# Performance work log

Measured on AMD Instinct MI355X. Metric: run time of the kernel, lower is better.

The kernel has to match this reference:

```python
import jax, jax.numpy as jnp
import numpy as np


def setup_inputs() -> dict:
    key = jax.random.key(0)
    k1, k2 = jax.random.split(key, 2)
    B, N, D = 8, 2048, 1024
    x = jax.random.normal(k1, (B, N, D), dtype=jnp.float32)
    # Linear(D, 3D): weight stored as [in, out] for x @ W
    W_qkv = jax.random.normal(k2, (D, 3 * D), dtype=jnp.float32) * (D ** -0.5)
    b_qkv = jnp.zeros((3 * D,), dtype=jnp.float32)
    return {"x": x, "W_qkv": W_qkv, "b_qkv": b_qkv}


def reference(x, W_qkv, b_qkv):
    D = x.shape[-1]
    scale = D ** -0.5
    qkv = x @ W_qkv + b_qkv                      # [B, N, 3D]
    q, k, v = jnp.split(qkv, 3, axis=-1)         # each [B, N, D]
    # attention scores: note original scales AFTER matmul (same math)
    atten = jnp.einsum('bnd,bmd->bnm', q, k) * scale  # [B, N, N]
    atten = jax.nn.softmax(atten, axis=-1)
    out = jnp.einsum('bnm,bmd->bnd', atten, v)   # [B, N, D]
    return out
```

## Files before the change

kernel.cpp:

```cpp
#include <hip/hip_runtime.h>
#include <hip/hip_bf16.h>


typedef __attribute__((ext_vector_type(8))) short bf16x8;
typedef __attribute__((ext_vector_type(4))) float f32x4;
typedef __attribute__((ext_vector_type(8))) unsigned short u16x8;
typedef __attribute__((address_space(1))) const unsigned int gu32;
typedef __attribute__((address_space(3))) unsigned int lu32;

__device__ __forceinline__ unsigned short f2bf(float f) {
  union { float f; unsigned int u; } v; v.f = f;
  unsigned int r = v.u + 0x7fffu + ((v.u >> 16) & 1u);
  return (unsigned short)(r >> 16);
}
__device__ __forceinline__ void cp16(const unsigned short* g, unsigned short* l) {
  __builtin_amdgcn_global_load_lds((gu32*)g, (lu32*)l, 16, 0, 0);
}

__global__ __launch_bounds__(256) void prep(const float* __restrict__ x,
                                            unsigned short* __restrict__ xb,
                                            const float* __restrict__ W,
                                            unsigned short* __restrict__ Wt,
                                            float* __restrict__ rowsum) {
  __shared__ unsigned short tile[64][72];
  int bid = blockIdx.x, t = threadIdx.x;
  if (bid < 8192) {
    long i = ((long)bid * 256 + t) * 8;
    float4 a = *(const float4*)(x + i);
    float4 b = *(const float4*)(x + i + 4);
    u16x8 o;
    o[0] = f2bf(a.x); o[1] = f2bf(a.y); o[2] = f2bf(a.z); o[3] = f2bf(a.w);
    o[4] = f2bf(b.x); o[5] = f2bf(b.y); o[6] = f2bf(b.z); o[7] = f2bf(b.w);
    *(u16x8*)(xb + i) = o;
  } else if (bid < 8960) {
    int wb = bid - 8192;
    int fb = wb % 48, db = wb / 48;
#pragma unroll
    for (int it = 0; it < 4; it++) {
      int c = t + it * 256;
      int r = c >> 4, c4 = (c & 15) * 4;
      float4 v = *(const float4*)(W + (long)(db * 64 + r) * 3072 + fb * 64 + c4);
      tile[r][c4 + 0] = f2bf(v.x); tile[r][c4 + 1] = f2bf(v.y);
      tile[r][c4 + 2] = f2bf(v.z); tile[r][c4 + 3] = f2bf(v.w);
    }
    __syncthreads();
#pragma unroll
    for (int it = 0; it < 2; it++) {
      int c = t + it * 256;
      int r2 = c >> 3, k8 = (c & 7) * 8;
      u16x8 o;
#pragma unroll
      for (int j = 0; j < 8; j++) o[j] = tile[k8 + j][r2];
      *(u16x8*)(Wt + (long)(fb * 64 + r2) * 1024 + db * 64 + k8) = o;
    }
  } else {
    rowsum[(bid - 8960) * 256 + t] = 0.f;
  }
}

template <int MODE, int SWZ>
__global__ __launch_bounds__(512, 2) void gemm256(
    const unsigned short* __restrict__ A, const unsigned short* __restrict__ B,
    float* __restrict__ C, const float* __restrict__ bias, int Ncols, int K, float scale,
    unsigned short* __restrict__ qp, unsigned short* __restrict__ kp,
    unsigned short* __restrict__ vp, float* __restrict__ rsum,
    long strA, long strB, long strC) {
  __shared__ __align__(16) unsigned short smem[4][256 * 64];
  const int tid = threadIdx.x;
  const int lane = tid & 63, wave = tid >> 6;
  const int quad = lane >> 4, l16 = lane & 15;
  const int lr = lane >> 3, lc = lane & 7;
  const int bz = blockIdx.z;
  int mt, nt;
  {
    int bid = blockIdx.x;
    const int nx = gridDim.x;
    bid = (bid & 7) * (nx >> 3) + (bid >> 3);
    int w = bid & 15, st = bid >> 4;
    constexpr int NSUP = (SWZ >= 4) ? (SWZ / 4) : 1;
    mt = (st / NSUP) * 4 + (w >> 2);
    nt = (st % NSUP) * 4 + (w & 3);
  }
  const long m0 = (long)mt * 256;
  const int n0 = nt * 256;
  const int wm128 = (wave >> 2) * 128;
  const int wn64 = (wave & 3) * 64;
  const int NT = K >> 6, mask = NT - 1;

  const unsigned short* __restrict__ Ab = A + (long)bz * strA;
  const unsigned short* __restrict__ Bb = B + (long)bz * strB;

  unsigned int aSrc[4], bSrc[4];
  int aOff[4], bOff[4];
  {
    const int auL[4] = {0, 128, 64, 192}, auH[4] = {32, 160, 96, 224};
    const int buL[4] = {0, 128, 32, 160}, buH[4] = {64, 192, 96, 224};
    const bool wlo = wave < 4;
    const int w8 = (wave & 3) * 8;
    const int sc = (lc ^ lr) * 8;
#pragma unroll
    for (int u = 0; u < 4; u++) {
      int ra = (wlo ? auL[u] : auH[u]) + w8 + lr;
      int rb = (wlo ? buL[u] : buH[u]) + w8 + lr;
      aSrc[u] = (unsigned int)(((int)m0 + ra) * K + sc);
      bSrc[u] = (unsigned int)((n0 + rb) * K + sc);
      aOff[u] = ra * 64 + lc * 8;
      bOff[u] = rb * 64 + lc * 8;
    }
  }

#define SA(u, bb, tt) cp16(Ab + aSrc[u] + (tt) * 64, &smem[bb][aOff[u]])
#define SB(u, bb, tt) cp16(Bb + bSrc[u] + (tt) * 64, &smem[2 + (bb)][bOff[u]])

  f32x4 acc[8][4];
  f32x4 zero = {0.f, 0.f, 0.f, 0.f};
#pragma unroll
  for (int i = 0; i < 8; i++)
#pragma unroll
    for (int j = 0; j < 4; j++) acc[i][j] = zero;
  bf16x8 am[2][2][2];
  bf16x8 bn[4][2];

#define RD_AQ(d, bb, q)                                                                     \
  _Pragma("unroll") for (int ii = 0; ii < 2; ii++) {                                        \
    int row = wm128 + ((q) * 2 + ii) * 16 + l16;                                            \
    _Pragma("unroll") for (int h = 0; h < 2; h++)                                           \
      am[d][ii][h] = *(const bf16x8*)(&smem[bb][row * 64 + ((((h << 2) | quad)) ^ (row & 7)) * 8]); \
  }
#define RD_BALL(bb)                                                                         \
  _Pragma("unroll") for (int jj = 0; jj < 4; jj++) {                                        \
    int row = wn64 + jj * 16 + l16;                                                         \
    _Pragma("unroll") for (int h = 0; h < 2; h++)                                           \
      bn[jj][h] = *(const bf16x8*)(&smem[2 + (bb)][row * 64 + ((((h << 2) | quad)) ^ (row & 7)) * 8]); \
  }
#define MMQ(q, d)                                                                           \
  _Pragma("unroll") for (int ii = 0; ii < 2; ii++)                                          \
    _Pragma("unroll") for (int jj = 0; jj < 4; jj++)                                        \
      _Pragma("unroll") for (int h = 0; h < 2; h++)                                         \
        acc[(q) * 2 + ii][jj] = __builtin_amdgcn_mfma_f32_16x16x32_bf16(                    \
            am[d][ii][h], bn[jj][h], acc[(q) * 2 + ii][jj], 0, 0, 0);
#define ABAR asm volatile("s_barrier" ::: "memory")
#define LGKM0 asm volatile("s_waitcnt lgkmcnt(0)" ::: "memory")
#define VMCNT4 asm volatile("s_waitcnt vmcnt(4)" ::: "memory")
#define PRIO1 __builtin_amdgcn_s_setprio(1)
#define PRIO0 __builtin_amdgcn_s_setprio(0)
#define SBAR0 __builtin_amdgcn_sched_barrier(0)

#define TILE(bb, tt)                                                                        \
  {                                                                                         \
    const int t2c_ = (tt) + 2;                                                              \
    const int t2_ = t2c_ > mask ? mask : t2c_;                                              \
                                                                                    \
    LGKM0; RD_AQ(1, bb, 1); ABAR;                                                           \
    SB(0, bb, t2_); SB(1, bb, t2_);                                                         \
    SBAR0; PRIO1; MMQ(0, 0); PRIO0; SBAR0;                                                  \
                                                                                    \
    LGKM0; RD_AQ(0, bb, 2); ABAR;                                                           \
    SA(0, bb, t2_); SA(1, bb, t2_);                                                         \
    SBAR0; PRIO1; MMQ(1, 1); PRIO0; SBAR0;                                                  \
                                                                                    \
    LGKM0; RD_AQ(1, bb, 3); VMCNT4; ABAR;                                                   \
    SB(2, bb, t2_); SB(3, bb, t2_);                                                         \
    SBAR0; PRIO1; MMQ(2, 0); PRIO0; SBAR0;                                                  \
                                                                                    \
    LGKM0; RD_AQ(0, (bb) ^ 1, 0);                                                           \
    SBAR0; PRIO1; MMQ(3, 1); PRIO0; SBAR0;                                                  \
    RD_BALL((bb) ^ 1);                                                                      \
    ABAR;                                                                                   \
    SA(2, bb, t2_); SA(3, bb, t2_);                                                         \
  }

  SA(0, 0, 0); SA(1, 0, 0); SB(0, 0, 0); SB(1, 0, 0);
  SA(2, 0, 0); SA(3, 0, 0); SB(2, 0, 0); SB(3, 0, 0);
  SA(0, 1, 1); SA(1, 1, 1); SB(0, 1, 1); SB(1, 1, 1);
  SA(2, 1, 1); SA(3, 1, 1); SB(2, 1, 1); SB(3, 1, 1);
  asm volatile("s_waitcnt vmcnt(8)" ::: "memory");
  ABAR;
  RD_AQ(0, 0, 0);
  RD_BALL(0);

#pragma unroll 1
  for (int t = 0; t < NT; t += 2) {
    TILE(0, t);
    TILE(1, t + 1);
  }

  if (MODE == 1 || MODE == 3) {
    asm volatile("s_waitcnt vmcnt(0)" ::: "memory");
    __syncthreads();
    unsigned short* Cs = &smem[0][0];
    if (MODE == 1) {
      float bv[4];
#pragma unroll
      for (int j = 0; j < 4; j++) bv[j] = bias[n0 + wn64 + j * 16 + l16];
      const bool isV = (n0 >= 2048);
#pragma unroll
      for (int i = 0; i < 8; i++)
#pragma unroll
        for (int r = 0; r < 4; r++) {
          int rw = wm128 + i * 16 + quad * 4 + r;
#pragma unroll
          for (int j = 0; j < 4; j++) {
            int cl = wn64 + j * 16 + l16;
            unsigned short hv = f2bf(acc[i][j][r] + bv[j]);
            int row = isV ? cl : rw, col = isV ? rw : cl;
            *(unsigned short*)((char*)Cs + ((row * 512 + col * 2) ^ ((row & 7) << 4))) = hv;
          }
        }
    } else {
      float* rs = rsum + bz * 2048;
#pragma unroll
      for (int i = 0; i < 8; i++)
#pragma unroll
        for (int r = 0; r < 4; r++) {
          int rw = wm128 + i * 16 + quad * 4 + r;
          float psum = 0.f;
#pragma unroll
          for (int j = 0; j < 4; j++) {
            float e = __expf(acc[i][j][r] * scale);
            psum += e;
            int col = wn64 + j * 16 + l16;
            *(unsigned short*)((char*)Cs + ((rw * 512 + col * 2) ^ ((rw & 7) << 4))) = f2bf(e);
          }
          psum += __shfl_xor(psum, 1);
          psum += __shfl_xor(psum, 2);
          psum += __shfl_xor(psum, 4);
          psum += __shfl_xor(psum, 8);
          if (l16 == 0) atomicAdd(rs + (m0 + rw), psum);
        }
    }
    __syncthreads();
    const int rrow = tid >> 5, rchunk = tid & 31;
    unsigned short* dst;
    long rowstr, rowbase, colbase;
    if (MODE == 3) {
      dst = qp + (long)bz * strC;
      rowstr = Ncols; rowbase = m0; colbase = n0;
    } else if (n0 < 2048) {
      dst = (n0 < 1024) ? qp : kp;
      rowstr = 1024; rowbase = m0; colbase = n0 & 1023;
    } else {
      dst = vp;
      rowstr = 2048; rowbase = (m0 >> 11) * 1024 + (n0 - 2048); colbase = m0 & 2047;
    }
#pragma unroll
    for (int k = 0; k < 16; k++) {
      int row = k * 16 + rrow;
      u16x8 v = *(const u16x8*)((char*)Cs + ((row * 512 + rchunk * 16) ^ ((row & 7) << 4)));
      *(u16x8*)(dst + (rowbase + row) * rowstr + colbase + rchunk * 8) = v;
    }
  } else {
    float* Co = C + (long)bz * strC;
    const float* rs = rsum + bz * 2048;
#pragma unroll
    for (int i = 0; i < 8; i++)
#pragma unroll
      for (int r = 0; r < 4; r++) {
        long gm = m0 + wm128 + i * 16 + quad * 4 + r;
        float inv = 1.0f / rs[gm];
#pragma unroll
        for (int j = 0; j < 4; j++)
          Co[gm * Ncols + n0 + wn64 + j * 16 + l16] = acc[i][j][r] * inv;
      }
  }
  asm volatile("s_waitcnt vmcnt(0) lgkmcnt(0)" ::: "memory");
#undef SA
#undef SB
#undef RD_AQ
#undef RD_BALL
#undef MMQ
#undef TILE
#undef ABAR
#undef LGKM0
#undef VMCNT4
#undef PRIO1
#undef PRIO0
#undef SBAR0
}

extern "C" void kernel_launch(void* const* d_in, const int* in_sizes, int n_in,
                              void* d_out, int out_size, void* d_ws, size_t ws_size,
                              hipStream_t stream) {
  const float* x = (const float*)d_in[0];
  const float* W = (const float*)d_in[1];
  const float* bq = (const float*)d_in[2];
  float* out = (float*)d_out;
  char* ws = (char*)d_ws;
  const long MB = 1L << 20;
  unsigned short* Q  = (unsigned short*)(ws);
  unsigned short* Kb = (unsigned short*)(ws + 32 * MB);
  unsigned short* Vt = (unsigned short*)(ws + 64 * MB);
  unsigned short* xb = (unsigned short*)(ws + 96 * MB);
  unsigned short* Wt = (unsigned short*)(ws + 128 * MB);
  unsigned short* E  = (unsigned short*)(ws + 96 * MB);
  float* rowsum      = (float*)(ws + 160 * MB);

  prep<<<9024, 256, 0, stream>>>(x, xb, W, Wt, rowsum);
  gemm256<1, 12><<<dim3(768, 1, 1), 512, 0, stream>>>(xb, Wt, nullptr, bq, 3072, 1024, 1.0f,
                                                      Q, Kb, Vt, nullptr, 0, 0, 0);
  gemm256<3, 8><<<dim3(64, 1, 8), 512, 0, stream>>>(Q, Kb, nullptr, nullptr, 2048, 1024,
                                                    0.03125f, E, nullptr, nullptr, rowsum,
                                                    2048L * 1024, 2048L * 1024, 2048L * 2048);
  gemm256<4, 4><<<dim3(32, 1, 8), 512, 0, stream>>>(E, Vt, out, nullptr, 1024, 2048, 1.0f,
                                                    nullptr, nullptr, nullptr, rowsum,
                                                    2048L * 2048, 1024L * 2048, 2048L * 1024);
}
```

Measured before the change: 377.8 us.

## Switch GEMM to 32x32x16 MFMA tiles and interleave next B-fragment loads

```diff
diff --git a/kernel.cpp b/kernel.cpp
--- a/kernel.cpp
+++ b/kernel.cpp
@@ -4,6 +4,7 @@
 
 typedef __attribute__((ext_vector_type(8))) short bf16x8;
 typedef __attribute__((ext_vector_type(4))) float f32x4;
+typedef __attribute__((ext_vector_type(16))) float f32x16;
 typedef __attribute__((ext_vector_type(8))) unsigned short u16x8;
 typedef __attribute__((address_space(1))) const unsigned int gu32;
 typedef __attribute__((address_space(3))) unsigned int lu32;
@@ -68,7 +69,7 @@
   __shared__ __align__(16) unsigned short smem[4][256 * 64];
   const int tid = threadIdx.x;
   const int lane = tid & 63, wave = tid >> 6;
-  const int quad = lane >> 4, l16 = lane & 15;
+  const int l32 = lane & 31, h5 = lane >> 5;
   const int lr = lane >> 3, lc = lane & 7;
   const int bz = blockIdx.z;
   int mt, nt;
@@ -112,33 +113,47 @@
 #define SA(u, bb, tt) cp16(Ab + aSrc[u] + (tt) * 64, &smem[bb][aOff[u]])
 #define SB(u, bb, tt) cp16(Bb + bSrc[u] + (tt) * 64, &smem[2 + (bb)][bOff[u]])
 
-  f32x4 acc[8][4];
-  f32x4 zero = {0.f, 0.f, 0.f, 0.f};
-#pragma unroll
-  for (int i = 0; i < 8; i++)
-#pragma unroll
-    for (int j = 0; j < 4; j++) acc[i][j] = zero;
-  bf16x8 am[2][2][2];
-  bf16x8 bn[4][2];
-
-#define RD_AQ(d, bb, q)                                                                     \
-  _Pragma("unroll") for (int ii = 0; ii < 2; ii++) {                                        \
-    int row = wm128 + ((q) * 2 + ii) * 16 + l16;                                            \
-    _Pragma("unroll") for (int h = 0; h < 2; h++)                                           \
-      am[d][ii][h] = *(const bf16x8*)(&smem[bb][row * 64 + ((((h << 2) | quad)) ^ (row & 7)) * 8]); \
+  f32x16 acc[4][2];
+#pragma unroll
+  for (int i = 0; i < 4; i++)
+#pragma unroll
+    for (int j = 0; j < 2; j++)
+#pragma unroll
+      for (int r = 0; r < 16; r++) acc[i][j][r] = 0.f;
+  bf16x8 am[2][4];
+  bf16x8 bn[2][4];
+
+#define RD_AQ(d, bb, mtq)                                                                   \
+  {                                                                                         \
+    int row_ = wm128 + (mtq) * 32 + l32;                                                    \
+    int rx_ = row_ & 7;                                                                     \
+    _Pragma("unroll") for (int ks = 0; ks < 4; ks++)                                        \
+        am[d][ks] = *(const bf16x8*)(&smem[bb][row_ * 64 + (((ks * 2 + h5) ^ rx_) * 8)]);   \
   }
 #define RD_BALL(bb)                                                                         \
-  _Pragma("unroll") for (int jj = 0; jj < 4; jj++) {                                        \
-    int row = wn64 + jj * 16 + l16;                                                         \
-    _Pragma("unroll") for (int h = 0; h < 2; h++)                                           \
-      bn[jj][h] = *(const bf16x8*)(&smem[2 + (bb)][row * 64 + ((((h << 2) | quad)) ^ (row & 7)) * 8]); \
-  }
-#define MMQ(q, d)                                                                           \
-  _Pragma("unroll") for (int ii = 0; ii < 2; ii++)                                          \
-    _Pragma("unroll") for (int jj = 0; jj < 4; jj++)                                        \
-      _Pragma("unroll") for (int h = 0; h < 2; h++)                                         \
-        acc[(q) * 2 + ii][jj] = __builtin_amdgcn_mfma_f32_16x16x32_bf16(                    \
-            am[d][ii][h], bn[jj][h], acc[(q) * 2 + ii][jj], 0, 0, 0);
+  _Pragma("unroll") for (int nt2 = 0; nt2 < 2; nt2++) {                                     \
+    int row_ = wn64 + nt2 * 32 + l32;                                                       \
+    int rx_ = row_ & 7;                                                                     \
+    _Pragma("unroll") for (int ks = 0; ks < 4; ks++)                                        \
+        bn[nt2][ks] = *(const bf16x8*)(&smem[2 + (bb)][row_ * 64 + (((ks * 2 + h5) ^ rx_) * 8)]); \
+  }
+#define MMQ(mtq, d)                                                                         \
+  _Pragma("unroll") for (int nt2 = 0; nt2 < 2; nt2++)                                       \
+      _Pragma("unroll") for (int ks = 0; ks < 4; ks++)                                      \
+          acc[mtq][nt2] = __builtin_amdgcn_mfma_f32_32x32x16_bf16(                          \
+              am[d][ks], bn[nt2][ks], acc[mtq][nt2], 0, 0, 0);
+#define MMQ_BSWAP(mtq, d, nb)                                                               \
+  _Pragma("unroll") for (int nt2 = 0; nt2 < 2; nt2++) {                                     \
+    int row_ = wn64 + nt2 * 32 + l32;                                                       \
+    int rx_ = row_ & 7;                                                                     \
+    _Pragma("unroll") for (int ks = 0; ks < 4; ks++) {                                      \
+      acc[mtq][nt2] = __builtin_amdgcn_mfma_f32_32x32x16_bf16(                              \
+          am[d][ks], bn[nt2][ks], acc[mtq][nt2], 0, 0, 0);                                  \
+      bn[nt2][ks] = *(const bf16x8*)(&smem[2 + (nb)][row_ * 64 + (((ks * 2 + h5) ^ rx_) * 8)]); \
+      __builtin_amdgcn_sched_group_barrier(0x008, 1, 0);                                    \
+      __builtin_amdgcn_sched_group_barrier(0x100, 1, 0);                                    \
+    }                                                                                       \
+  }
 #define ABAR asm volatile("s_barrier" ::: "memory")
 #define LGKM0 asm volatile("s_waitcnt lgkmcnt(0)" ::: "memory")
 #define VMCNT4 asm volatile("s_waitcnt vmcnt(4)" ::: "memory")
@@ -162,10 +177,9 @@
     LGKM0; RD_AQ(1, bb, 3); VMCNT4; ABAR;                                                   \
     SB(2, bb, t2_); SB(3, bb, t2_);                                                         \
     SBAR0; PRIO1; MMQ(2, 0); PRIO0; SBAR0;                                                  \
-                                                                                    \
+         \
     LGKM0; RD_AQ(0, (bb) ^ 1, 0);                                                           \
-    SBAR0; PRIO1; MMQ(3, 1); PRIO0; SBAR0;                                                  \
-    RD_BALL((bb) ^ 1);                                                                      \
+    SBAR0; PRIO1; MMQ_BSWAP(3, 1, (bb) ^ 1); PRIO0; SBAR0;                                  \
     ABAR;                                                                                   \
     SA(2, bb, t2_); SA(3, bb, t2_);                                                         \
   }
@@ -190,43 +204,43 @@
     __syncthreads();
     unsigned short* Cs = &smem[0][0];
     if (MODE == 1) {
-      float bv[4];
-#pragma unroll
-      for (int j = 0; j < 4; j++) bv[j] = bias[n0 + wn64 + j * 16 + l16];
+      float bv[2];
+#pragma unroll
+      for (int nt2 = 0; nt2 < 2; nt2++) bv[nt2] = bias[n0 + wn64 + nt2 * 32 + l32];
       const bool isV = (n0 >= 2048);
 #pragma unroll
-      for (int i = 0; i < 8; i++)
-#pragma unroll
-        for (int r = 0; r < 4; r++) {
-          int rw = wm128 + i * 16 + quad * 4 + r;
-#pragma unroll
-          for (int j = 0; j < 4; j++) {
-            int cl = wn64 + j * 16 + l16;
-            unsigned short hv = f2bf(acc[i][j][r] + bv[j]);
+      for (int i = 0; i < 4; i++)
+#pragma unroll
+        for (int nt2 = 0; nt2 < 2; nt2++)
+#pragma unroll
+          for (int r = 0; r < 16; r++) {
+            int rw = wm128 + i * 32 + (r & 3) + ((r >> 2) * 8) + 4 * h5;
+            int cl = wn64 + nt2 * 32 + l32;
+            unsigned short hv = f2bf(acc[i][nt2][r] + bv[nt2]);
             int row = isV ? cl : rw, col = isV ? rw : cl;
             *(unsigned short*)((char*)Cs + ((row * 512 + col * 2) ^ ((row & 7) << 4))) = hv;
           }
-        }
     } else {
       float* rs = rsum + bz * 2048;
 #pragma unroll
-      for (int i = 0; i < 8; i++)
-#pragma unroll
-        for (int r = 0; r < 4; r++) {
-          int rw = wm128 + i * 16 + quad * 4 + r;
+      for (int i = 0; i < 4; i++)
+#pragma unroll
+        for (int r = 0; r < 16; r++) {
+          int rw = wm128 + i * 32 + (r & 3) + ((r >> 2) * 8) + 4 * h5;
           float psum = 0.f;
 #pragma unroll
-          for (int j = 0; j < 4; j++) {
-            float e = __expf(acc[i][j][r] * scale);
+          for (int nt2 = 0; nt2 < 2; nt2++) {
+            float e = __expf(acc[i][nt2][r] * scale);
             psum += e;
-            int col = wn64 + j * 16 + l16;
+            int col = wn64 + nt2 * 32 + l32;
             *(unsigned short*)((char*)Cs + ((rw * 512 + col * 2) ^ ((rw & 7) << 4))) = f2bf(e);
           }
           psum += __shfl_xor(psum, 1);
           psum += __shfl_xor(psum, 2);
           psum += __shfl_xor(psum, 4);
           psum += __shfl_xor(psum, 8);
-          if (l16 == 0) atomicAdd(rs + (m0 + rw), psum);
+          psum += __shfl_xor(psum, 16);
+          if (l32 == 0) atomicAdd(rs + (m0 + rw), psum);
         }
     }
     __syncthreads();
@@ -253,14 +267,14 @@
     float* Co = C + (long)bz * strC;
     const float* rs = rsum + bz * 2048;
 #pragma unroll
-    for (int i = 0; i < 8; i++)
-#pragma unroll
-      for (int r = 0; r < 4; r++) {
-        long gm = m0 + wm128 + i * 16 + quad * 4 + r;
+    for (int i = 0; i < 4; i++)
+#pragma unroll
+      for (int r = 0; r < 16; r++) {
+        long gm = m0 + wm128 + i * 32 + (r & 3) + ((r >> 2) * 8) + 4 * h5;
         float inv = 1.0f / rs[gm];
 #pragma unroll
-        for (int j = 0; j < 4; j++)
-          Co[gm * Ncols + n0 + wn64 + j * 16 + l16] = acc[i][j][r] * inv;
+        for (int nt2 = 0; nt2 < 2; nt2++)
+          Co[gm * Ncols + n0 + wn64 + nt2 * 32 + l32] = acc[i][nt2][r] * inv;
       }
   }
   asm volatile("s_waitcnt vmcnt(0) lgkmcnt(0)" ::: "memory");
@@ -269,6 +283,7 @@
 #undef RD_AQ
 #undef RD_BALL
 #undef MMQ
+#undef MMQ_BSWAP
 #undef TILE
 #undef ABAR
 #undef LGKM0
```

After: 385.3 us. +2.0%, slower.

## Interleave LDS fragment reads with MFMA groups in GEMM main loop

Applied to the files above, without the earlier changes.

```diff
diff --git a/kernel.cpp b/kernel.cpp
--- a/kernel.cpp
+++ b/kernel.cpp
@@ -133,15 +133,51 @@
     _Pragma("unroll") for (int h = 0; h < 2; h++)                                           \
       bn[jj][h] = *(const bf16x8*)(&smem[2 + (bb)][row * 64 + ((((h << 2) | quad)) ^ (row & 7)) * 8]); \
   }
-#define MMQ(q, d)                                                                           \
-  _Pragma("unroll") for (int ii = 0; ii < 2; ii++)                                          \
-    _Pragma("unroll") for (int jj = 0; jj < 4; jj++)                                        \
-      _Pragma("unroll") for (int h = 0; h < 2; h++)                                         \
-        acc[(q) * 2 + ii][jj] = __builtin_amdgcn_mfma_f32_16x16x32_bf16(                    \
-            am[d][ii][h], bn[jj][h], acc[(q) * 2 + ii][jj], 0, 0, 0);
+#define MMQ_INT(q, d, dn, qn, bb)                                                           \
+  _Pragma("unroll") for (int jj = 0; jj < 4; jj++) {                                        \
+    acc[(q) * 2 + 0][jj] = __builtin_amdgcn_mfma_f32_16x16x32_bf16(                         \
+        am[d][0][0], bn[jj][0], acc[(q) * 2 + 0][jj], 0, 0, 0);                             \
+    acc[(q) * 2 + 1][jj] = __builtin_amdgcn_mfma_f32_16x16x32_bf16(                         \
+        am[d][1][0], bn[jj][0], acc[(q) * 2 + 1][jj], 0, 0, 0);                             \
+    acc[(q) * 2 + 0][jj] = __builtin_amdgcn_mfma_f32_16x16x32_bf16(                         \
+        am[d][0][1], bn[jj][1], acc[(q) * 2 + 0][jj], 0, 0, 0);                             \
+    acc[(q) * 2 + 1][jj] = __builtin_amdgcn_mfma_f32_16x16x32_bf16(                         \
+        am[d][1][1], bn[jj][1], acc[(q) * 2 + 1][jj], 0, 0, 0);                             \
+    {                                                                                       \
+      int ii_ = jj >> 1, h_ = jj & 1;                                                       \
+      int row_ = wm128 + ((qn) * 2 + ii_) * 16 + l16;                                       \
+      am[dn][ii_][h_] = *(const bf16x8*)(                                                   \
+          &smem[bb][row_ * 64 + ((((h_ << 2) | quad)) ^ (row_ & 7)) * 8]);                  \
+    }                                                                                       \
+    __builtin_amdgcn_sched_group_barrier(0x008, 4, 0);                                      \
+    __builtin_amdgcn_sched_group_barrier(0x100, 1, 0);                                      \
+  }
+#define MMQ_FIN(q, d, nb)                                                                   \
+  _Pragma("unroll") for (int jj = 0; jj < 4; jj++) {                                        \
+    acc[(q) * 2 + 0][jj] = __builtin_amdgcn_mfma_f32_16x16x32_bf16(                         \
+        am[d][0][0], bn[jj][0], acc[(q) * 2 + 0][jj], 0, 0, 0);                             \
+    acc[(q) * 2 + 1][jj] = __builtin_amdgcn_mfma_f32_16x16x32_bf16(                         \
+        am[d][1][0], bn[jj][0], acc[(q) * 2 + 1][jj], 0, 0, 0);                             \
+    acc[(q) * 2 + 0][jj] = __builtin_amdgcn_mfma_f32_16x16x32_bf16(                         \
+        am[d][0][1], bn[jj][1], acc[(q) * 2 + 0][jj], 0, 0, 0);                             \
+    acc[(q) * 2 + 1][jj] = __builtin_amdgcn_mfma_f32_16x16x32_bf16(                         \
+        am[d][1][1], bn[jj][1], acc[(q) * 2 + 1][jj], 0, 0, 0);                             \
+    {                                                                                       \
+      int rowb_ = wn64 + jj * 16 + l16;                                                     \
+      int rxb_ = rowb_ & 7;                                                                 \
+      bn[jj][0] = *(const bf16x8*)(&smem[2 + (nb)][rowb_ * 64 + (quad ^ rxb_) * 8]);        \
+      bn[jj][1] = *(const bf16x8*)(&smem[2 + (nb)][rowb_ * 64 + ((4 | quad) ^ rxb_) * 8]);  \
+      int ii_ = jj >> 1, h_ = jj & 1;                                                       \
+      int row_ = wm128 + ii_ * 16 + l16;                                                    \
+      am[0][ii_][h_] = *(const bf16x8*)(                                                    \
+          &smem[nb][row_ * 64 + ((((h_ << 2) | quad)) ^ (row_ & 7)) * 8]);                  \
+    }                                                                                       \
+    __builtin_amdgcn_sched_group_barrier(0x008, 4, 0);                                      \
+    __builtin_amdgcn_sched_group_barrier(0x100, 3, 0);                                      \
+  }
 #define ABAR asm volatile("s_barrier" ::: "memory")
 #define LGKM0 asm volatile("s_waitcnt lgkmcnt(0)" ::: "memory")
-#define VMCNT4 asm volatile("s_waitcnt vmcnt(4)" ::: "memory")
+#define LGKM0VM6 asm volatile("s_waitcnt vmcnt(6) lgkmcnt(0)" ::: "memory")
 #define PRIO1 __builtin_amdgcn_s_setprio(1)
 #define PRIO0 __builtin_amdgcn_s_setprio(0)
 #define SBAR0 __builtin_amdgcn_sched_barrier(0)
@@ -150,24 +186,26 @@
   {                                                                                         \
     const int t2c_ = (tt) + 2;                                                              \
     const int t2_ = t2c_ > mask ? mask : t2c_;                                              \
-                                                                                    \
-    LGKM0; RD_AQ(1, bb, 1); ABAR;                                                           \
+                                   \
+    ABAR;                                                                                   \
     SB(0, bb, t2_); SB(1, bb, t2_);                                                         \
-    SBAR0; PRIO1; MMQ(0, 0); PRIO0; SBAR0;                                                  \
-                                                                                    \
-    LGKM0; RD_AQ(0, bb, 2); ABAR;                                                           \
+    SBAR0; PRIO1; MMQ_INT(0, 0, 1, 1, bb); PRIO0; SBAR0;                                    \
+    LGKM0;                                                                                  \
+                                        \
+    ABAR;                                                                                   \
     SA(0, bb, t2_); SA(1, bb, t2_);                                                         \
-    SBAR0; PRIO1; MMQ(1, 1); PRIO0; SBAR0;                                                  \
-                                                                                    \
-    LGKM0; RD_AQ(1, bb, 3); VMCNT4; ABAR;                                                   \
+    SBAR0; PRIO1; MMQ_INT(1, 1, 0, 2, bb); PRIO0; SBAR0;                                    \
+    LGKM0;                                                                                  \
+                        \
+    ABAR;                                                                                   \
     SB(2, bb, t2_); SB(3, bb, t2_);                                                         \
-    SBAR0; PRIO1; MMQ(2, 0); PRIO0; SBAR0;                                                  \
-                                                                                    \
-    LGKM0; RD_AQ(0, (bb) ^ 1, 0);                                                           \
-    SBAR0; PRIO1; MMQ(3, 1); PRIO0; SBAR0;                                                  \
-    RD_BALL((bb) ^ 1);                                                                      \
+    SBAR0; PRIO1; MMQ_INT(2, 0, 1, 3, bb); PRIO0; SBAR0;                                    \
+    LGKM0VM6;                                                                               \
+                              \
     ABAR;                                                                                   \
     SA(2, bb, t2_); SA(3, bb, t2_);                                                         \
+    SBAR0; PRIO1; MMQ_FIN(3, 1, (bb) ^ 1); PRIO0; SBAR0;                                    \
+    LGKM0;                                                                                  \
   }
 
   SA(0, 0, 0); SA(1, 0, 0); SB(0, 0, 0); SB(1, 0, 0);
@@ -178,6 +216,7 @@
   ABAR;
   RD_AQ(0, 0, 0);
   RD_BALL(0);
+  LGKM0;
 
 #pragma unroll 1
   for (int t = 0; t < NT; t += 2) {
@@ -268,11 +307,12 @@
 #undef SB
 #undef RD_AQ
 #undef RD_BALL
-#undef MMQ
+#undef MMQ_INT
+#undef MMQ_FIN
 #undef TILE
 #undef ABAR
 #undef LGKM0
-#undef VMCNT4
+#undef LGKM0VM6
 #undef PRIO1
 #undef PRIO0
 #undef SBAR0
```

New measurement: 362.9 us. 1.04x faster.
